# Kernel optimization log

Measured on AMD Instinct MI355X. Metric: run time of the kernel, lower is better.

## Reference

```python
import jax, jax.numpy as jnp
import numpy as np

B, S, D, H = 32, 8192, 128, 256  # batch-of-MLPs, seq_len, emb_dim, hidden_dim
LN_EPS = 1e-5


def setup_inputs() -> dict:
    key = jax.random.key(0)
    k0, k1, k2, k3 = jax.random.split(key, 4)
    x = jax.random.normal(k0, (B, S, D), dtype=jnp.float32)
    # shared learned Q projection (torch Linear stores W as [out,in]; y = x @ W.T)
    Wq = jax.random.normal(k1, (D, D), dtype=jnp.float32) / np.float32(np.sqrt(D))
    # per-batch-index (non-shared) fast-weight MLP params
    W1 = jax.random.normal(k2, (B, D, H), dtype=jnp.float32) / np.float32(np.sqrt(D))
    b1 = jnp.zeros((B, H), dtype=jnp.float32)
    W2 = jax.random.normal(k3, (B, H, D), dtype=jnp.float32) / np.float32(np.sqrt(H))
    b2 = jnp.zeros((B, D), dtype=jnp.float32)
    gamma = jnp.ones((B, D), dtype=jnp.float32)
    beta = jnp.zeros((B, D), dtype=jnp.float32)
    return dict(x=x, Wq=Wq, W1=W1, b1=b1, W2=W2, b2=b2, gamma=gamma, beta=beta)


def reference(x, Wq, W1, b1, W2, b2, gamma, beta):
    # queries = silu(Q(x))
    q = jax.nn.silu(jnp.einsum('bsd,ed->bse', x, Wq))
    # torch F.normalize with default dim=1 -> L2-normalize over the sequence axis
    q = q / jnp.clip(jnp.linalg.norm(q, axis=1, keepdims=True), 1e-12)
    # ParallelMLPs: per-index MLP with distinct weights (grouped GEMM), + residual
    h = jax.nn.silu(jnp.einsum('bsd,bdh->bsh', q, W1) + b1[:, None, :])
    o = jnp.einsum('bsh,bhd->bsd', h, W2) + b2[:, None, :]
    mu = jnp.mean(o, axis=-1, keepdims=True)
    var = jnp.mean(jnp.square(o - mu), axis=-1, keepdims=True)
    ln = (o - mu) / jnp.sqrt(var + LN_EPS) * gamma[:, None, :] + beta[:, None, :]
    return ln + q
```

## Files before the change

kernel.cpp:

```cpp
#include <hip/hip_runtime.h>
#include <stdint.h>

#define B_ 32
#define S_ 8192
#define D_ 128
#define H_ 256

typedef __attribute__((ext_vector_type(4))) float f32x4;
typedef __attribute__((ext_vector_type(16))) float f32x16;
typedef __attribute__((ext_vector_type(8))) short bf16x8;
typedef __attribute__((ext_vector_type(4))) unsigned int u32x4;

__device__ __forceinline__ unsigned short f2bf(float f) {
    union { float f; unsigned int u; } v; v.f = f;
    unsigned int r = v.u + 0x7fffu + ((v.u >> 16) & 1u);
    return (unsigned short)(r >> 16);
}
__device__ __forceinline__ float bf2f(unsigned short u) {
    union { unsigned int u; float f; } v; v.u = ((unsigned int)u) << 16;
    return v.f;
}
__device__ __forceinline__ float silu_f(float v) {
    return v * __builtin_amdgcn_rcpf(1.0f + __expf(-v));
}
__device__ __forceinline__ unsigned int cvtpk(float lo, float hi) {
    unsigned int r;
    asm("v_cvt_pk_bf16_f32 %0, %1, %2" : "=v"(r) : "v"(lo), "v"(hi));
    return r;
}
__device__ __forceinline__ void plswap(unsigned int& a, unsigned int& b) {
    asm("v_permlane32_swap_b32 %0, %1" : "+v"(a), "+v"(b));
}

__global__ void k_prep(const float* __restrict__ Wq, const float* __restrict__ W1,
                       const float* __restrict__ W2, const float* __restrict__ b1,
                       unsigned short* __restrict__ wq_bf,
                       unsigned short* __restrict__ w1s,
                       unsigned short* __restrict__ w2s,
                       float* __restrict__ b1r) {
    __shared__ __align__(16) unsigned short tile[8192];
    int t = threadIdx.x, blk = blockIdx.x;
    if (blk < 128) {
        int b = blk >> 2, hc = blk & 3;
#pragma unroll
        for (int i = 0; i < 8; i++) {
            int idx = t + i * 256;
            int d = idx >> 4, hj = idx & 15;
            f32x4 v = *(const f32x4*)(W1 + ((size_t)(b * D_ + d)) * H_ + hc * 64 + hj * 4);
#pragma unroll
            for (int u = 0; u < 4; u++) tile[(hj * 4 + u) * 128 + d] = f2bf(v[u]);
        }
        __syncthreads();
        char* img = (char*)w1s + (size_t)blk * 16384;
#pragma unroll
        for (int i = 0; i < 4; i++) {
            int c = t + i * 256;
            int n = c >> 9, kk = (c >> 6) & 7, l = c & 63;
            u32x4 v = *(const u32x4*)(tile + (n * 32 + (l & 31)) * 128 + kk * 16 + (l >> 5) * 8);
            *(u32x4*)(img + c * 16) = v;
        }
    } else if (blk < 256) {
        int a = blk - 128;
        int b = a >> 2, hc = a & 3;
#pragma unroll
        for (int i = 0; i < 8; i++) {
            int idx = t + i * 256;
            int h = idx >> 5, d4 = idx & 31;
            f32x4 v = *(const f32x4*)(W2 + ((size_t)(b * H_ + hc * 64 + h)) * D_ + d4 * 4);
#pragma unroll
            for (int u = 0; u < 4; u++) tile[(d4 * 4 + u) * 64 + h] = f2bf(v[u]);
        }
        __syncthreads();
        char* img = (char*)w2s + (size_t)a * 16384;
#pragma unroll
        for (int i = 0; i < 4; i++) {
            int c = t + i * 256;
            int dn = c >> 8, n = (c >> 7) & 1, kk2 = (c >> 6) & 1, l = c & 63;
            u32x4 v = *(const u32x4*)(tile + (dn * 32 + (l & 31)) * 64 + n * 32 + kk2 * 16 + (l >> 5) * 8);
            *(u32x4*)(img + c * 16) = v;
        }
    } else if (blk < 320) {
        int i = (blk - 256) * 256 + t;
        wq_bf[i] = f2bf(Wq[i]);
    } else {
        int idx = (blk - 320) * 256 + t;
        int b = idx >> 8, rem = idx & 255;
        int hc = rem >> 6, n = (rem >> 5) & 1, hi = (rem >> 4) & 1, r = rem & 15;
        int h = hc * 64 + n * 32 + (r & 3) + 8 * (r >> 2) + 4 * hi;
        b1r[idx] = b1[b * H_ + h];
    }
}

__global__ __launch_bounds__(256, 2) void k_qproj(
        const float* __restrict__ x, const unsigned short* __restrict__ wq_bf,
        unsigned short* __restrict__ q_img, float* __restrict__ part) {
    __shared__ __align__(16) unsigned short lds_a[128 * 128];
    __shared__ __align__(16) unsigned short lds_b[128 * 128];
    __shared__ float lds_ss[4][128];

    int tid = threadIdx.x;
    int lane = tid & 63, w = tid >> 6;
    int g = lane >> 4, c15 = lane & 15;
    int blk = blockIdx.x;
    int b = blk >> 6, st = blk & 63;
    size_t rowbase = (size_t)b * S_ + (size_t)st * 128;
    const float* xg = x + rowbase * D_;

    char* pA = (char*)lds_a;
    char* pB = (char*)lds_b;

#pragma unroll
    for (int i = 0; i < 8; i++) {
        int idx = tid + i * 256;
        int row = idx >> 4, cb = idx & 15;
        u32x4 v = *(const u32x4*)(wq_bf + row * 128 + cb * 8);
        *(u32x4*)(pB + row * 256 + (((unsigned)cb ^ (unsigned)(row & 7)) << 4)) = v;
    }
#pragma unroll
    for (int i = 0; i < 16; i++) {
        int idx = tid + i * 256;
        int row = idx >> 5, c4 = idx & 31;
        f32x4 v = *(const f32x4*)(xg + (size_t)row * 128 + c4 * 4);
        unsigned int lo = cvtpk(v[0], v[1]), hi2 = cvtpk(v[2], v[3]);
        *(unsigned long long*)(pA + row * 256 + ((c4 * 8) ^ ((row & 7) << 4))) =
            ((unsigned long long)hi2 << 32) | (unsigned long long)lo;
    }
    __syncthreads();

    f32x4 acc[2][8];
#pragma unroll
    for (int m = 0; m < 2; m++)
#pragma unroll
        for (int n = 0; n < 8; n++) acc[m][n] = (f32x4)0.0f;

#pragma unroll
    for (int kk = 0; kk < 4; kk++) {
        int kb = kk * 64 + (g << 4);
        bf16x8 a[2];
#pragma unroll
        for (int m = 0; m < 2; m++) {
            int row = (w << 5) + (m << 4) + c15;
            a[m] = *(const bf16x8*)(pA + row * 256 + (kb ^ ((row & 7) << 4)));
        }
#pragma unroll
        for (int n = 0; n < 8; n++) {
            int rowb = (n << 4) + c15;
            bf16x8 bb = *(const bf16x8*)(pB + rowb * 256 + (kb ^ ((rowb & 7) << 4)));
#pragma unroll
            for (int m = 0; m < 2; m++)
                acc[m][n] = __builtin_amdgcn_mfma_f32_16x16x32_bf16(a[m], bb, acc[m][n], 0, 0, 0);
        }
    }

    float ss[8];
#pragma unroll
    for (int n = 0; n < 8; n++) ss[n] = 0.0f;
#pragma unroll
    for (int m = 0; m < 2; m++)
#pragma unroll
        for (int n = 0; n < 8; n++)
#pragma unroll
            for (int r = 0; r < 4; r++) {
                float v = silu_f(acc[m][n][r]);
                acc[m][n][r] = v;
                ss[n] += v * v;
            }
#pragma unroll
    for (int n = 0; n < 8; n++) {
        float v = ss[n];
        v += __shfl_xor(v, 16, 64);
        v += __shfl_xor(v, 32, 64);
        if (lane < 16) lds_ss[w][(n << 4) + lane] = v;
    }
    __syncthreads();

#pragma unroll
    for (int m = 0; m < 2; m++)
#pragma unroll
        for (int n = 0; n < 8; n++)
#pragma unroll
            for (int r = 0; r < 4; r++) {
                int row = (w << 5) + (m << 4) + (g << 2) + r;
                int col = (n << 4) + c15;
                int byte = (row >> 5) * 8192 + (col >> 4) * 1024 +
                           ((row & 31) + ((col >> 3) & 1) * 32) * 16 + (col & 7) * 2;
                *(unsigned short*)(pA + byte) = f2bf(acc[m][n][r]);
            }
    __syncthreads();

    char* qo = (char*)q_img + ((size_t)(b * 256 + st * 4)) * 8192;
#pragma unroll
    for (int i = 0; i < 8; i++) {
        int off = tid * 16 + i * 4096;
        *(u32x4*)(qo + off) = *(const u32x4*)(pA + off);
    }
    if (tid < 128) {
        float s = lds_ss[0][tid] + lds_ss[1][tid] + lds_ss[2][tid] + lds_ss[3][tid];
        part[((size_t)b * 64 + st) * 128 + tid] = s;
    }
}

__global__ void k_scale(const float* __restrict__ part, float* __restrict__ scale) {
    int idx = blockIdx.x * 256 + threadIdx.x;
    int b = idx >> 7, e = idx & 127;
    const float* p = part + (size_t)b * 64 * 128 + e;
    float s = 0.0f;
    for (int t = 0; t < 64; t++) s += p[t * 128];
    scale[idx] = 1.0f / fmaxf(sqrtf(s), 1e-12f);
}

__global__ void k_wscale(unsigned short* __restrict__ w1s, const float* __restrict__ scale) {
    int blk = blockIdx.x;
    int b = blk >> 2;
    char* region = (char*)w1s + (size_t)blk * 16384;
    int t = threadIdx.x;
#pragma unroll
    for (int i = 0; i < 4; i++) {
        int c = t + i * 256;
        int kk = (c >> 6) & 7, l = c & 63;
        int d0 = kk * 16 + (l >> 5) * 8;
        u32x4 v = *(const u32x4*)(region + c * 16);
        const unsigned short* pv = (const unsigned short*)&v;
        const float* sc = scale + b * D_ + d0;
        u32x4 o;
#pragma unroll
        for (int j = 0; j < 4; j++)
            o[j] = cvtpk(bf2f(pv[2 * j]) * sc[2 * j], bf2f(pv[2 * j + 1]) * sc[2 * j + 1]);
        *(u32x4*)(region + c * 16) = o;
    }
}

__global__ __launch_bounds__(256, 2) void k_mlp(
        const unsigned short* __restrict__ q_img, const float* __restrict__ scale,
        const unsigned short* __restrict__ w1s, const unsigned short* __restrict__ w2s,
        const float* __restrict__ b1r, const float* __restrict__ b2,
        const float* __restrict__ gamma, const float* __restrict__ beta,
        float* __restrict__ out) {
    __shared__ __align__(16) char lds[32768];
    int tid = threadIdx.x;
    int lane = tid & 63, w = tid >> 6;
    int c31 = lane & 31, hi = lane >> 5;
    int blk = blockIdx.x;
    int k = blk & 7, j = blk >> 3;
    int b = k * 4 + (j >> 6);
    int st = j & 63;

    const char* w1b = (const char*)w1s + (size_t)(b * 4) * 16384;
    const char* w2b = (const char*)w2s + (size_t)(b * 4) * 16384;
    size_t grp = (size_t)(b * 256 + st * 4 + w);
    const char* qg = (const char*)q_img + grp * 8192;

    bf16x8 qf[8];
#pragma unroll
    for (int kk = 0; kk < 8; kk++)
        qf[kk] = *(const bf16x8*)(qg + kk * 1024 + lane * 16);

    char* myq = (char*)lds + w * 8192;
#pragma unroll
    for (int kk = 0; kk < 8; kk++)
        *(bf16x8*)(myq + c31 * 256 + ((kk * 32 + hi * 16) ^ ((c31 & 7) << 4))) = qf[kk];

    f32x16 acco[4];
#pragma unroll
    for (int dn = 0; dn < 4; dn++)
#pragma unroll
        for (int e = 0; e < 16; e++) acco[dn][e] = 0.0f;

#pragma unroll
    for (int hc = 0; hc < 4; hc++) {
        const char* w1h = w1b + hc * 16384;
        const char* w2h = w2b + hc * 16384;
#pragma unroll
        for (int n = 0; n < 2; n++) {
            const float* b1p = b1r + ((b * 4 + hc) * 2 + n) * 32 + hi * 16;
            f32x16 acch;
#pragma unroll
            for (int jq = 0; jq < 4; jq++) {
                f32x4 bq = *(const f32x4*)(b1p + jq * 4);
#pragma unroll
                for (int e = 0; e < 4; e++) acch[jq * 4 + e] = bq[e];
            }
#pragma unroll
            for (int kk = 0; kk < 8; kk++) {
                bf16x8 wf = *(const bf16x8*)(w1h + n * 8192 + kk * 1024 + lane * 16);
                acch = __builtin_amdgcn_mfma_f32_32x32x16_bf16(wf, qf[kk], acch, 0, 0, 0);
            }
            float sv[16];
#pragma unroll
            for (int r = 0; r < 16; r++) sv[r] = silu_f(acch[r]);
            unsigned int P[8];
#pragma unroll
            for (int p = 0; p < 8; p++) P[p] = cvtpk(sv[2 * p], sv[2 * p + 1]);
            plswap(P[0], P[2]); plswap(P[1], P[3]);
            plswap(P[4], P[6]); plswap(P[5], P[7]);
            union { unsigned int u[4]; bf16x8 v; } f0, f1;
            f0.u[0] = P[0]; f0.u[1] = P[1]; f0.u[2] = P[2]; f0.u[3] = P[3];
            f1.u[0] = P[4]; f1.u[1] = P[5]; f1.u[2] = P[6]; f1.u[3] = P[7];
            bf16x8 pa0 = f0.v, pa1 = f1.v;
#pragma unroll
            for (int dn = 0; dn < 4; dn++) {
                bf16x8 wf20 = *(const bf16x8*)(w2h + dn * 4096 + n * 2048 + lane * 16);
                bf16x8 wf21 = *(const bf16x8*)(w2h + dn * 4096 + n * 2048 + 1024 + lane * 16);
                acco[dn] = __builtin_amdgcn_mfma_f32_32x32x16_bf16(pa0, wf20, acco[dn], 0, 0, 0);
                acco[dn] = __builtin_amdgcn_mfma_f32_32x32x16_bf16(pa1, wf21, acco[dn], 0, 0, 0);
            }
        }
    }

    float scv[4], gv[4], bev[4], b2v[4];
#pragma unroll
    for (int dn = 0; dn < 4; dn++) {
        int d = dn * 32 + c31;
        scv[dn] = scale[b * 128 + d];
        gv[dn]  = gamma[b * 128 + d];
        bev[dn] = beta[b * 128 + d];
        b2v[dn] = b2[b * 128 + d];
    }

    float* og = out + grp * 32 * 128;
#pragma unroll
    for (int r = 0; r < 16; r++) {
        float v0 = acco[0][r] + b2v[0], v1 = acco[1][r] + b2v[1];
        float v2 = acco[2][r] + b2v[2], v3 = acco[3][r] + b2v[3];
        float s1 = (v0 + v1) + (v2 + v3);
        float s2 = (v0 * v0 + v1 * v1) + (v2 * v2 + v3 * v3);
        s1 += __shfl_xor(s1, 1, 64);   s2 += __shfl_xor(s2, 1, 64);
        s1 += __shfl_xor(s1, 2, 64);   s2 += __shfl_xor(s2, 2, 64);
        s1 += __shfl_xor(s1, 4, 64);   s2 += __shfl_xor(s2, 4, 64);
        s1 += __shfl_xor(s1, 8, 64);   s2 += __shfl_xor(s2, 8, 64);
        s1 += __shfl_xor(s1, 16, 64);  s2 += __shfl_xor(s2, 16, 64);
        float mu = s1 * (1.0f / 128.0f);
        float var = s2 * (1.0f / 128.0f) - mu * mu;
        float rstd = rsqrtf(var + 1e-5f);
        int srow0 = (r & 3) + 8 * (r >> 2);
        int row = srow0 + 4 * hi;
        float vv[4] = {v0, v1, v2, v3};
#pragma unroll
        for (int dn = 0; dn < 4; dn++) {
            float qv = bf2f(*(const unsigned short*)(myq + row * 256 +
                        ((dn * 64 + c31 * 2) ^ ((row & 7) << 4)))) * scv[dn];
            float o = (vv[dn] - mu) * rstd * gv[dn] + bev[dn] + qv;
            og[(size_t)row * 128 + dn * 32 + c31] = o;
        }
    }
}

extern "C" void kernel_launch(void* const* d_in, const int* in_sizes, int n_in,
                              void* d_out, int out_size, void* d_ws, size_t ws_size,
                              hipStream_t stream) {
    (void)in_sizes; (void)n_in; (void)out_size; (void)ws_size;
    const float* x     = (const float*)d_in[0];
    const float* Wq    = (const float*)d_in[1];
    const float* W1    = (const float*)d_in[2];
    const float* b1    = (const float*)d_in[3];
    const float* W2    = (const float*)d_in[4];
    const float* b2    = (const float*)d_in[5];
    const float* gamma = (const float*)d_in[6];
    const float* beta  = (const float*)d_in[7];
    float* out = (float*)d_out;

    char* ws = (char*)d_ws;
    unsigned short* wq_bf = (unsigned short*)(ws);
    unsigned short* w1s   = (unsigned short*)(ws + 32768);
    unsigned short* w2s   = (unsigned short*)(ws + 2129920);
    float* part           = (float*)(ws + 4227072);
    float* scale          = (float*)(ws + 5275648);
    float* b1r            = (float*)(ws + 5292032);
    unsigned short* q_img = (unsigned short*)(ws + 5324800);

    hipLaunchKernelGGL(k_prep, dim3(352), dim3(256), 0, stream, Wq, W1, W2, b1, wq_bf, w1s, w2s, b1r);
    hipLaunchKernelGGL(k_qproj, dim3(2048), dim3(256), 0, stream, x, wq_bf, q_img, part);
    hipLaunchKernelGGL(k_scale, dim3(16), dim3(256), 0, stream, part, scale);
    hipLaunchKernelGGL(k_wscale, dim3(128), dim3(256), 0, stream, w1s, scale);
    hipLaunchKernelGGL(k_mlp, dim3(2048), dim3(256), 0, stream,
                       q_img, scale, w1s, w2s, b1r, b2, gamma, beta, out);
}
```

Baseline: 153.1 us.

## Stage per-batch W1 in LDS via direct global-to-LDS loads; persistent 512-thread blocks

The MLP kernel now launches 512 blocks of 512 threads. Each block loads the whole 64KB W1 slice for its batch into LDS with global_load_lds, then each wave processes two 32-row groups in a loop, reading W1 fragments from LDS instead of global or L2. The aim is to cut repeated global weight traffic and give more reuse per block. In exchange, 128KB of LDS per block limits occupancy to one block per CU, and there is an upfront load-then-barrier stall. W2 is still read from global memory.

Result: slower. 272.0 us (+77.6%).

```diff
diff --git a/kernel.cpp b/kernel.cpp
--- a/kernel.cpp
+++ b/kernel.cpp
@@ -30,6 +30,11 @@
 }
 __device__ __forceinline__ void plswap(unsigned int& a, unsigned int& b) {
     asm("v_permlane32_swap_b32 %0, %1" : "+v"(a), "+v"(b));
+}
+__device__ __forceinline__ void gl16(const void* g, void* l) {
+    __builtin_amdgcn_global_load_lds(
+        (const __attribute__((address_space(1))) unsigned int*)g,
+        (__attribute__((address_space(3))) unsigned int*)l, 16, 0, 0);
 }
 
 __global__ void k_prep(const float* __restrict__ Wq, const float* __restrict__ W1,
@@ -230,81 +235,29 @@
     }
 }
 
-__global__ __launch_bounds__(256, 2) void k_mlp(
+__global__ __launch_bounds__(512, 1) void k_mlp(
         const unsigned short* __restrict__ q_img, const float* __restrict__ scale,
         const unsigned short* __restrict__ w1s, const unsigned short* __restrict__ w2s,
         const float* __restrict__ b1r, const float* __restrict__ b2,
         const float* __restrict__ gamma, const float* __restrict__ beta,
         float* __restrict__ out) {
-    __shared__ __align__(16) char lds[32768];
+    __shared__ __align__(16) char lds[131072];
     int tid = threadIdx.x;
     int lane = tid & 63, w = tid >> 6;
     int c31 = lane & 31, hi = lane >> 5;
-    int blk = blockIdx.x;
-    int k = blk & 7, j = blk >> 3;
-    int b = k * 4 + (j >> 6);
-    int st = j & 63;
-
-    const char* w1b = (const char*)w1s + (size_t)(b * 4) * 16384;
-    const char* w2b = (const char*)w2s + (size_t)(b * 4) * 16384;
-    size_t grp = (size_t)(b * 256 + st * 4 + w);
-    const char* qg = (const char*)q_img + grp * 8192;
-
-    bf16x8 qf[8];
-#pragma unroll
-    for (int kk = 0; kk < 8; kk++)
-        qf[kk] = *(const bf16x8*)(qg + kk * 1024 + lane * 16);
-
-    char* myq = (char*)lds + w * 8192;
-#pragma unroll
-    for (int kk = 0; kk < 8; kk++)
-        *(bf16x8*)(myq + c31 * 256 + ((kk * 32 + hi * 16) ^ ((c31 & 7) << 4))) = qf[kk];
-
-    f32x16 acco[4];
-#pragma unroll
-    for (int dn = 0; dn < 4; dn++)
-#pragma unroll
-        for (int e = 0; e < 16; e++) acco[dn][e] = 0.0f;
-
-#pragma unroll
-    for (int hc = 0; hc < 4; hc++) {
-        const char* w1h = w1b + hc * 16384;
-        const char* w2h = w2b + hc * 16384;
-#pragma unroll
-        for (int n = 0; n < 2; n++) {
-            const float* b1p = b1r + ((b * 4 + hc) * 2 + n) * 32 + hi * 16;
-            f32x16 acch;
-#pragma unroll
-            for (int jq = 0; jq < 4; jq++) {
-                f32x4 bq = *(const f32x4*)(b1p + jq * 4);
-#pragma unroll
-                for (int e = 0; e < 4; e++) acch[jq * 4 + e] = bq[e];
-            }
-#pragma unroll
-            for (int kk = 0; kk < 8; kk++) {
-                bf16x8 wf = *(const bf16x8*)(w1h + n * 8192 + kk * 1024 + lane * 16);
-                acch = __builtin_amdgcn_mfma_f32_32x32x16_bf16(wf, qf[kk], acch, 0, 0, 0);
-            }
-            float sv[16];
-#pragma unroll
-            for (int r = 0; r < 16; r++) sv[r] = silu_f(acch[r]);
-            unsigned int P[8];
-#pragma unroll
-            for (int p = 0; p < 8; p++) P[p] = cvtpk(sv[2 * p], sv[2 * p + 1]);
-            plswap(P[0], P[2]); plswap(P[1], P[3]);
-            plswap(P[4], P[6]); plswap(P[5], P[7]);
-            union { unsigned int u[4]; bf16x8 v; } f0, f1;
-            f0.u[0] = P[0]; f0.u[1] = P[1]; f0.u[2] = P[2]; f0.u[3] = P[3];
-            f1.u[0] = P[4]; f1.u[1] = P[5]; f1.u[2] = P[6]; f1.u[3] = P[7];
-            bf16x8 pa0 = f0.v, pa1 = f1.v;
-#pragma unroll
-            for (int dn = 0; dn < 4; dn++) {
-                bf16x8 wf20 = *(const bf16x8*)(w2h + dn * 4096 + n * 2048 + lane * 16);
-                bf16x8 wf21 = *(const bf16x8*)(w2h + dn * 4096 + n * 2048 + 1024 + lane * 16);
-                acco[dn] = __builtin_amdgcn_mfma_f32_32x32x16_bf16(pa0, wf20, acco[dn], 0, 0, 0);
-                acco[dn] = __builtin_amdgcn_mfma_f32_32x32x16_bf16(pa1, wf21, acco[dn], 0, 0, 0);
-            }
-        }
+    int id = blockIdx.x;
+    int xcd = id & 7, l = id >> 3;
+    int b = xcd * 4 + (l & 3);
+    int g = l >> 2;
+    int wv = g * 8 + w;
+
+    const char* w1b = (const char*)w1s + (size_t)b * 65536;
+    const char* w2b = (const char*)w2s + (size_t)b * 65536;
+
+#pragma unroll
+    for (int i = 0; i < 8; i++) {
+        int off = tid * 16 + i * 8192;
+        gl16(w1b + off, lds + off);
     }
 
     float scv[4], gv[4], bev[4], b2v[4];
@@ -317,30 +270,94 @@
         b2v[dn] = b2[b * 128 + d];
     }
 
-    float* og = out + grp * 32 * 128;
-#pragma unroll
-    for (int r = 0; r < 16; r++) {
-        float v0 = acco[0][r] + b2v[0], v1 = acco[1][r] + b2v[1];
-        float v2 = acco[2][r] + b2v[2], v3 = acco[3][r] + b2v[3];
-        float s1 = (v0 + v1) + (v2 + v3);
-        float s2 = (v0 * v0 + v1 * v1) + (v2 * v2 + v3 * v3);
-        s1 += __shfl_xor(s1, 1, 64);   s2 += __shfl_xor(s2, 1, 64);
-        s1 += __shfl_xor(s1, 2, 64);   s2 += __shfl_xor(s2, 2, 64);
-        s1 += __shfl_xor(s1, 4, 64);   s2 += __shfl_xor(s2, 4, 64);
-        s1 += __shfl_xor(s1, 8, 64);   s2 += __shfl_xor(s2, 8, 64);
-        s1 += __shfl_xor(s1, 16, 64);  s2 += __shfl_xor(s2, 16, 64);
-        float mu = s1 * (1.0f / 128.0f);
-        float var = s2 * (1.0f / 128.0f) - mu * mu;
-        float rstd = rsqrtf(var + 1e-5f);
-        int srow0 = (r & 3) + 8 * (r >> 2);
-        int row = srow0 + 4 * hi;
-        float vv[4] = {v0, v1, v2, v3};
-#pragma unroll
-        for (int dn = 0; dn < 4; dn++) {
-            float qv = bf2f(*(const unsigned short*)(myq + row * 256 +
-                        ((dn * 64 + c31 * 2) ^ ((row & 7) << 4)))) * scv[dn];
-            float o = (vv[dn] - mu) * rstd * gv[dn] + bev[dn] + qv;
-            og[(size_t)row * 128 + dn * 32 + c31] = o;
+    char* myq = (char*)lds + 65536 + w * 8192;
+    __syncthreads();
+
+#pragma unroll 1
+    for (int t = 0; t < 2; t++) {
+        size_t grp = (size_t)b * 256 + (size_t)(wv + 128 * t);
+        const char* qg = (const char*)q_img + grp * 8192;
+
+        bf16x8 qf[8];
+#pragma unroll
+        for (int kk = 0; kk < 8; kk++)
+            qf[kk] = *(const bf16x8*)(qg + kk * 1024 + lane * 16);
+
+#pragma unroll
+        for (int kk = 0; kk < 8; kk++)
+            *(bf16x8*)(myq + c31 * 256 + ((kk * 32 + hi * 16) ^ ((c31 & 7) << 4))) = qf[kk];
+
+        f32x16 acco[4];
+#pragma unroll
+        for (int dn = 0; dn < 4; dn++)
+#pragma unroll
+            for (int e = 0; e < 16; e++) acco[dn][e] = 0.0f;
+
+#pragma unroll
+        for (int hc = 0; hc < 4; hc++) {
+            const char* w2h = w2b + hc * 16384;
+#pragma unroll
+            for (int n = 0; n < 2; n++) {
+                const float* b1p = b1r + ((b * 4 + hc) * 2 + n) * 32 + hi * 16;
+                f32x16 acch;
+#pragma unroll
+                for (int jq = 0; jq < 4; jq++) {
+                    f32x4 bq = *(const f32x4*)(b1p + jq * 4);
+#pragma unroll
+                    for (int e = 0; e < 4; e++) acch[jq * 4 + e] = bq[e];
+                }
+#pragma unroll
+                for (int kk = 0; kk < 8; kk++) {
+                    bf16x8 wf = *(const bf16x8*)(lds + hc * 16384 + n * 8192 + kk * 1024 + lane * 16);
+                    acch = __builtin_amdgcn_mfma_f32_32x32x16_bf16(wf, qf[kk], acch, 0, 0, 0);
+                }
+                float sv[16];
+#pragma unroll
+                for (int r = 0; r < 16; r++) sv[r] = silu_f(acch[r]);
+                unsigned int P[8];
+#pragma unroll
+                for (int p = 0; p < 8; p++) P[p] = cvtpk(sv[2 * p], sv[2 * p + 1]);
+                plswap(P[0], P[2]); plswap(P[1], P[3]);
+                plswap(P[4], P[6]); plswap(P[5], P[7]);
+                union { unsigned int u[4]; bf16x8 v; } f0, f1;
+                f0.u[0] = P[0]; f0.u[1] = P[1]; f0.u[2] = P[2]; f0.u[3] = P[3];
+                f1.u[0] = P[4]; f1.u[1] = P[5]; f1.u[2] = P[6]; f1.u[3] = P[7];
+                bf16x8 pa0 = f0.v, pa1 = f1.v;
+#pragma unroll
+                for (int dn = 0; dn < 4; dn++) {
+                    bf16x8 wf20 = *(const bf16x8*)(w2h + dn * 4096 + n * 2048 + lane * 16);
+                    bf16x8 wf21 = *(const bf16x8*)(w2h + dn * 4096 + n * 2048 + 1024 + lane * 16);
+                    acco[dn] = __builtin_amdgcn_mfma_f32_32x32x16_bf16(pa0, wf20, acco[dn], 0, 0, 0);
+                    acco[dn] = __builtin_amdgcn_mfma_f32_32x32x16_bf16(pa1, wf21, acco[dn], 0, 0, 0);
+                }
+            }
+        }
+
+        float* og = out + grp * 32 * 128;
+#pragma unroll
+        for (int r = 0; r < 16; r++) {
+            float v0 = acco[0][r] + b2v[0], v1 = acco[1][r] + b2v[1];
+            float v2 = acco[2][r] + b2v[2], v3 = acco[3][r] + b2v[3];
+            float s1 = (v0 + v1) + (v2 + v3);
+            float s2 = (v0 * v0 + v1 * v1) + (v2 * v2 + v3 * v3);
+            s1 += __shfl_xor(s1, 1, 64);   s2 += __shfl_xor(s2, 1, 64);
+            s1 += __shfl_xor(s1, 2, 64);   s2 += __shfl_xor(s2, 2, 64);
+            s1 += __shfl_xor(s1, 4, 64);   s2 += __shfl_xor(s2, 4, 64);
+            s1 += __shfl_xor(s1, 8, 64);   s2 += __shfl_xor(s2, 8, 64);
+            s1 += __shfl_xor(s1, 16, 64);  s2 += __shfl_xor(s2, 16, 64);
+            float mu = s1 * (1.0f / 128.0f);
+            float var = s2 * (1.0f / 128.0f) - mu * mu;
+            float rstd = rsqrtf(var + 1e-5f);
+            int srow0 = (r & 3) + 8 * (r >> 2);
+            int row = srow0 + 4 * hi;
+            float vv[4] = {v0, v1, v2, v3};
+#pragma unroll
+            for (int dn = 0; dn < 4; dn++) {
+                float qv = bf2f(*(const unsigned short*)(myq + row * 256 +
+                            ((dn * 64 + c31 * 2) ^ ((row & 7) << 4)))) * scv[dn];
+                float o = (vv[dn] - mu) * rstd * gv[dn] + bev[dn] + qv;
+                og[(size_t)row * 128 + dn * 32 + c31] = o;
+            }
         }
     }
 }
@@ -372,6 +389,6 @@
     hipLaunchKernelGGL(k_qproj, dim3(2048), dim3(256), 0, stream, x, wq_bf, q_img, part);
     hipLaunchKernelGGL(k_scale, dim3(16), dim3(256), 0, stream, part, scale);
     hipLaunchKernelGGL(k_wscale, dim3(128), dim3(256), 0, stream, w1s, scale);
-    hipLaunchKernelGGL(k_mlp, dim3(2048), dim3(256), 0, stream,
+    hipLaunchKernelGGL(k_mlp, dim3(512), dim3(512), 0, stream,
                        q_img, scale, w1s, w2s, b1r, b2, gamma, beta, out);
 }
```

## Stage interleaved W1/W2 packages into LDS with double-buffered async loads

Applied to the files above, without the earlier changes.

Repacks W1 and W2 into one interleaved per-batch package, so each 16KB chunk holds the W1 and W2 slices for one hidden sub-block. The MLP kernel then streams these chunks into two LDS slots with global_load_lds and computes from LDS instead of each wave reading the weights from global memory. Each workgroup shares the weight loads across its four waves and overlaps the next chunk's load with compute. This adds barriers per stage and slightly more LDS use, which could limit occupancy at two blocks per CU.

Measured after the change: 132.7 us. -13.3%, faster.

```diff
diff --git a/kernel.cpp b/kernel.cpp
--- a/kernel.cpp
+++ b/kernel.cpp
@@ -31,12 +31,16 @@
 __device__ __forceinline__ void plswap(unsigned int& a, unsigned int& b) {
     asm("v_permlane32_swap_b32 %0, %1" : "+v"(a), "+v"(b));
 }
+__device__ __forceinline__ void gl16(const void* g, void* l) {
+    __builtin_amdgcn_global_load_lds(
+        (const __attribute__((address_space(1))) unsigned int*)g,
+        (__attribute__((address_space(3))) unsigned int*)l, 16, 0, 0);
+}
 
 __global__ void k_prep(const float* __restrict__ Wq, const float* __restrict__ W1,
                        const float* __restrict__ W2, const float* __restrict__ b1,
                        unsigned short* __restrict__ wq_bf,
-                       unsigned short* __restrict__ w1s,
-                       unsigned short* __restrict__ w2s,
+                       unsigned short* __restrict__ wpkg,
                        float* __restrict__ b1r) {
     __shared__ __align__(16) unsigned short tile[8192];
     int t = threadIdx.x, blk = blockIdx.x;
@@ -51,13 +55,13 @@
             for (int u = 0; u < 4; u++) tile[(hj * 4 + u) * 128 + d] = f2bf(v[u]);
         }
         __syncthreads();
-        char* img = (char*)w1s + (size_t)blk * 16384;
+        char* img = (char*)wpkg + (size_t)b * 131072 + (size_t)hc * 32768;
 #pragma unroll
         for (int i = 0; i < 4; i++) {
             int c = t + i * 256;
             int n = c >> 9, kk = (c >> 6) & 7, l = c & 63;
             u32x4 v = *(const u32x4*)(tile + (n * 32 + (l & 31)) * 128 + kk * 16 + (l >> 5) * 8);
-            *(u32x4*)(img + c * 16) = v;
+            *(u32x4*)(img + n * 16384 + kk * 1024 + l * 16) = v;
         }
     } else if (blk < 256) {
         int a = blk - 128;
@@ -71,13 +75,13 @@
             for (int u = 0; u < 4; u++) tile[(d4 * 4 + u) * 64 + h] = f2bf(v[u]);
         }
         __syncthreads();
-        char* img = (char*)w2s + (size_t)a * 16384;
+        char* img = (char*)wpkg + (size_t)b * 131072 + (size_t)hc * 32768;
 #pragma unroll
         for (int i = 0; i < 4; i++) {
             int c = t + i * 256;
             int dn = c >> 8, n = (c >> 7) & 1, kk2 = (c >> 6) & 1, l = c & 63;
             u32x4 v = *(const u32x4*)(tile + (dn * 32 + (l & 31)) * 64 + n * 32 + kk2 * 16 + (l >> 5) * 8);
-            *(u32x4*)(img + c * 16) = v;
+            *(u32x4*)(img + n * 16384 + 8192 + dn * 2048 + kk2 * 1024 + l * 16) = v;
         }
     } else if (blk < 320) {
         int i = (blk - 256) * 256 + t;
@@ -209,34 +213,34 @@
     scale[idx] = 1.0f / fmaxf(sqrtf(s), 1e-12f);
 }
 
-__global__ void k_wscale(unsigned short* __restrict__ w1s, const float* __restrict__ scale) {
+__global__ void k_wscale(unsigned short* __restrict__ wpkg, const float* __restrict__ scale) {
     int blk = blockIdx.x;
     int b = blk >> 2;
-    char* region = (char*)w1s + (size_t)blk * 16384;
+    char* region = (char*)wpkg + (size_t)b * 131072 + (size_t)(blk & 3) * 32768;
     int t = threadIdx.x;
 #pragma unroll
     for (int i = 0; i < 4; i++) {
         int c = t + i * 256;
-        int kk = (c >> 6) & 7, l = c & 63;
+        int n = c >> 9, kk = (c >> 6) & 7, l = c & 63;
+        char* addr = region + n * 16384 + kk * 1024 + l * 16;
         int d0 = kk * 16 + (l >> 5) * 8;
-        u32x4 v = *(const u32x4*)(region + c * 16);
+        u32x4 v = *(const u32x4*)addr;
         const unsigned short* pv = (const unsigned short*)&v;
         const float* sc = scale + b * D_ + d0;
         u32x4 o;
 #pragma unroll
         for (int j = 0; j < 4; j++)
             o[j] = cvtpk(bf2f(pv[2 * j]) * sc[2 * j], bf2f(pv[2 * j + 1]) * sc[2 * j + 1]);
-        *(u32x4*)(region + c * 16) = o;
+        *(u32x4*)addr = o;
     }
 }
 
 __global__ __launch_bounds__(256, 2) void k_mlp(
         const unsigned short* __restrict__ q_img, const float* __restrict__ scale,
-        const unsigned short* __restrict__ w1s, const unsigned short* __restrict__ w2s,
-        const float* __restrict__ b1r, const float* __restrict__ b2,
-        const float* __restrict__ gamma, const float* __restrict__ beta,
-        float* __restrict__ out) {
-    __shared__ __align__(16) char lds[32768];
+        const unsigned short* __restrict__ wpkg, const float* __restrict__ b1r,
+        const float* __restrict__ b2, const float* __restrict__ gamma,
+        const float* __restrict__ beta, float* __restrict__ out) {
+    __shared__ __align__(16) char lds[33792];
     int tid = threadIdx.x;
     int lane = tid & 63, w = tid >> 6;
     int c31 = lane & 31, hi = lane >> 5;
@@ -245,9 +249,8 @@
     int b = k * 4 + (j >> 6);
     int st = j & 63;
 
-    const char* w1b = (const char*)w1s + (size_t)(b * 4) * 16384;
-    const char* w2b = (const char*)w2s + (size_t)(b * 4) * 16384;
-    size_t grp = (size_t)(b * 256 + st * 4 + w);
+    const char* wb = (const char*)wpkg + (size_t)b * 131072;
+    size_t grp = (size_t)b * 256 + st * 4 + w;
     const char* qg = (const char*)q_img + grp * 8192;
 
     bf16x8 qf[8];
@@ -255,57 +258,83 @@
     for (int kk = 0; kk < 8; kk++)
         qf[kk] = *(const bf16x8*)(qg + kk * 1024 + lane * 16);
 
+    gl16((const char*)b1r + (size_t)b * 1024 + lane * 16, lds + 32768);
+
+#define STAGEPKG(p, slot) do {                                          \
+    _Pragma("unroll")                                                   \
+    for (int i_ = 0; i_ < 4; i_++) {                                    \
+        int off_ = tid * 16 + i_ * 4096;                                \
+        gl16(wb + (p) * 16384 + off_, lds + (slot) * 16384 + off_);     \
+    } } while (0)
+
+    STAGEPKG(0, 0);
+    STAGEPKG(1, 1);
+
+    f32x16 acco[4];
+#pragma unroll
+    for (int dn = 0; dn < 4; dn++)
+#pragma unroll
+        for (int e = 0; e < 16; e++) acco[dn][e] = 0.0f;
+
+    const float* b1l = (const float*)(lds + 32768);
+
+#pragma unroll
+    for (int p = 0; p < 8; p++) {
+        const int hc = p >> 1, n = p & 1, slot = p & 1;
+        if (p == 7) { asm volatile("s_waitcnt vmcnt(0)" ::: "memory"); }
+        else        { asm volatile("s_waitcnt vmcnt(4)" ::: "memory"); }
+        __builtin_amdgcn_s_barrier();
+        __builtin_amdgcn_sched_barrier(0);
+
+        f32x16 acch;
+        {
+            const float* bp = b1l + (hc * 2 + n) * 32 + hi * 16;
+#pragma unroll
+            for (int jq = 0; jq < 4; jq++) {
+                f32x4 bq = *(const f32x4*)(bp + jq * 4);
+#pragma unroll
+                for (int e = 0; e < 4; e++) acch[jq * 4 + e] = bq[e];
+            }
+        }
+        const char* s0 = lds + slot * 16384;
+#pragma unroll
+        for (int kk = 0; kk < 8; kk++) {
+            bf16x8 wf = *(const bf16x8*)(s0 + kk * 1024 + lane * 16);
+            acch = __builtin_amdgcn_mfma_f32_32x32x16_bf16(wf, qf[kk], acch, 0, 0, 0);
+        }
+        float sv[16];
+#pragma unroll
+        for (int r = 0; r < 16; r++) sv[r] = silu_f(acch[r]);
+        unsigned int P[8];
+#pragma unroll
+        for (int pp = 0; pp < 8; pp++) P[pp] = cvtpk(sv[2 * pp], sv[2 * pp + 1]);
+        plswap(P[0], P[2]); plswap(P[1], P[3]);
+        plswap(P[4], P[6]); plswap(P[5], P[7]);
+        union { unsigned int u[4]; bf16x8 v; } f0, f1;
+        f0.u[0] = P[0]; f0.u[1] = P[1]; f0.u[2] = P[2]; f0.u[3] = P[3];
+        f1.u[0] = P[4]; f1.u[1] = P[5]; f1.u[2] = P[6]; f1.u[3] = P[7];
+        bf16x8 pa0 = f0.v, pa1 = f1.v;
+#pragma unroll
+        for (int kk2 = 0; kk2 < 2; kk2++)
+#pragma unroll
+            for (int dn = 0; dn < 4; dn++) {
+                bf16x8 wf2 = *(const bf16x8*)(s0 + 8192 + dn * 2048 + kk2 * 1024 + lane * 16);
+                acco[dn] = __builtin_amdgcn_mfma_f32_32x32x16_bf16(kk2 ? pa1 : pa0, wf2,
+                                                                   acco[dn], 0, 0, 0);
+            }
+
+        asm volatile("s_waitcnt lgkmcnt(0)" ::: "memory");
+        __builtin_amdgcn_sched_barrier(0);
+        __builtin_amdgcn_s_barrier();
+        if (p < 6) STAGEPKG(p + 2, slot);
+    }
+#undef STAGEPKG
+
+    __syncthreads();
     char* myq = (char*)lds + w * 8192;
 #pragma unroll
     for (int kk = 0; kk < 8; kk++)
         *(bf16x8*)(myq + c31 * 256 + ((kk * 32 + hi * 16) ^ ((c31 & 7) << 4))) = qf[kk];
-
-    f32x16 acco[4];
-#pragma unroll
-    for (int dn = 0; dn < 4; dn++)
-#pragma unroll
-        for (int e = 0; e < 16; e++) acco[dn][e] = 0.0f;
-
-#pragma unroll
-    for (int hc = 0; hc < 4; hc++) {
-        const char* w1h = w1b + hc * 16384;
-        const char* w2h = w2b + hc * 16384;
-#pragma unroll
-        for (int n = 0; n < 2; n++) {
-            const float* b1p = b1r + ((b * 4 + hc) * 2 + n) * 32 + hi * 16;
-            f32x16 acch;
-#pragma unroll
-            for (int jq = 0; jq < 4; jq++) {
-                f32x4 bq = *(const f32x4*)(b1p + jq * 4);
-#pragma unroll
-                for (int e = 0; e < 4; e++) acch[jq * 4 + e] = bq[e];
-            }
-#pragma unroll
-            for (int kk = 0; kk < 8; kk++) {
-                bf16x8 wf = *(const bf16x8*)(w1h + n * 8192 + kk * 1024 + lane * 16);
-                acch = __builtin_amdgcn_mfma_f32_32x32x16_bf16(wf, qf[kk], acch, 0, 0, 0);
-            }
-            float sv[16];
-#pragma unroll
-            for (int r = 0; r < 16; r++) sv[r] = silu_f(acch[r]);
-            unsigned int P[8];
-#pragma unroll
-            for (int p = 0; p < 8; p++) P[p] = cvtpk(sv[2 * p], sv[2 * p + 1]);
-            plswap(P[0], P[2]); plswap(P[1], P[3]);
-            plswap(P[4], P[6]); plswap(P[5], P[7]);
-            union { unsigned int u[4]; bf16x8 v; } f0, f1;
-            f0.u[0] = P[0]; f0.u[1] = P[1]; f0.u[2] = P[2]; f0.u[3] = P[3];
-            f1.u[0] = P[4]; f1.u[1] = P[5]; f1.u[2] = P[6]; f1.u[3] = P[7];
-            bf16x8 pa0 = f0.v, pa1 = f1.v;
-#pragma unroll
-            for (int dn = 0; dn < 4; dn++) {
-                bf16x8 wf20 = *(const bf16x8*)(w2h + dn * 4096 + n * 2048 + lane * 16);
-                bf16x8 wf21 = *(const bf16x8*)(w2h + dn * 4096 + n * 2048 + 1024 + lane * 16);
-                acco[dn] = __builtin_amdgcn_mfma_f32_32x32x16_bf16(pa0, wf20, acco[dn], 0, 0, 0);
-                acco[dn] = __builtin_amdgcn_mfma_f32_32x32x16_bf16(pa1, wf21, acco[dn], 0, 0, 0);
-            }
-        }
-    }
 
     float scv[4], gv[4], bev[4], b2v[4];
 #pragma unroll
@@ -361,17 +390,16 @@
 
     char* ws = (char*)d_ws;
     unsigned short* wq_bf = (unsigned short*)(ws);
-    unsigned short* w1s   = (unsigned short*)(ws + 32768);
-    unsigned short* w2s   = (unsigned short*)(ws + 2129920);
+    unsigned short* wpkg  = (unsigned short*)(ws + 32768);
     float* part           = (float*)(ws + 4227072);
     float* scale          = (float*)(ws + 5275648);
     float* b1r            = (float*)(ws + 5292032);
     unsigned short* q_img = (unsigned short*)(ws + 5324800);
 
-    hipLaunchKernelGGL(k_prep, dim3(352), dim3(256), 0, stream, Wq, W1, W2, b1, wq_bf, w1s, w2s, b1r);
+    hipLaunchKernelGGL(k_prep, dim3(352), dim3(256), 0, stream, Wq, W1, W2, b1, wq_bf, wpkg, b1r);
     hipLaunchKernelGGL(k_qproj, dim3(2048), dim3(256), 0, stream, x, wq_bf, q_img, part);
     hipLaunchKernelGGL(k_scale, dim3(16), dim3(256), 0, stream, part, scale);
-    hipLaunchKernelGGL(k_wscale, dim3(128), dim3(256), 0, stream, w1s, scale);
+    hipLaunchKernelGGL(k_wscale, dim3(128), dim3(256), 0, stream, wpkg, scale);
     hipLaunchKernelGGL(k_mlp, dim3(2048), dim3(256), 0, stream,
-                       q_img, scale, w1s, w2s, b1r, b2, gamma, beta, out);
-}
+                       q_img, scale, wpkg, b1r, b2, gamma, beta, out);
+}
```
